# Kernel optimization log

Measured on AMD Instinct MI355X. Metric: run time of the kernel, lower is better.

The kernel has to match this reference:

```python
import jax, jax.numpy as jnp
import numpy as np

# config constants (match init_kwargs)
C = 1024
NH = 16
HS = C // NH
CHUNK = 64          # attn_chunk_size
TOPK = 32           # attn_topk
WINDOW = 4096       # kv_cache_window_size
MIN_KV = 16384      # min_kv_cache_size
MAX_KV = 32768      # max_kv_cache_size
SHORT = 4096        # short_sequence_criteria
CT = 65536          # incoming kv-cache length


def setup_inputs() -> dict:
    key = jax.random.key(0)
    ks = jax.random.split(key, 7)
    s = 1.0 / np.sqrt(C)
    return {
        "x": jax.random.normal(ks[0], (C,), jnp.float32),
        "k_cache": jax.random.normal(ks[1], (1, CT, C), jnp.float32),
        "v_cache": jax.random.normal(ks[2], (1, CT, C), jnp.float32),
        "Wr": jax.random.normal(ks[3], (C, C), jnp.float32) * s,
        "Wk": jax.random.normal(ks[4], (C, C), jnp.float32) * s,
        "Wv": jax.random.normal(ks[5], (C, C), jnp.float32) * s,
        "Wo": jax.random.normal(ks[6], (C, C), jnp.float32) * s,
    }


def _split_heads(t):  # (1, T, C) -> (1, NH, T, HS)
    return t.reshape(1, t.shape[1], NH, HS).transpose(0, 2, 1, 3)


def _update_kv_cache(q, k_cache, v_cache):
    # q: (1,1,C); caches: (1,CT,C). CT > MIN_KV so compression runs.
    past = CT - WINDOW
    kp = _split_heads(k_cache[:, :past])          # (1,NH,past,HS)
    vp = _split_heads(v_cache[:, :past])
    qh = _split_heads(q)                          # (1,NH,1,HS)
    scores = jnp.einsum("bhqd,bhkd->bhqk", qh, kp) / np.sqrt(HS)
    w = jax.nn.softmax(scores, axis=-1)           # (1,NH,1,past)
    vote = w.sum(axis=-2)                         # (1,NH,past)
    keep = MIN_KV - WINDOW                        # per-head tokens kept
    _, idx = jax.lax.top_k(vote, keep)            # (1,NH,keep), descending vote order
    kpc = jnp.take_along_axis(kp, idx[..., None], axis=2)  # (1,NH,keep,HS)
    vpc = jnp.take_along_axis(vp, idx[..., None], axis=2)
    kpc = kpc.transpose(0, 2, 1, 3).reshape(1, keep, C)
    vpc = vpc.transpose(0, 2, 1, 3).reshape(1, keep, C)
    k_new = jnp.concatenate([kpc, k_cache[:, past:]], axis=1)  # (1, MIN_KV, C)
    v_new = jnp.concatenate([vpc, v_cache[:, past:]], axis=1)
    return k_new, v_new


def reference(x, k_cache, v_cache, Wr, Wk, Wv, Wo):
    x2 = x[None, None, :]                         # (1,1,C)
    q = x2 @ Wr.T
    k = x2 @ Wk.T
    v = x2 @ Wv.T

    # CT > MAX_KV -> compress cache (eviction via attention vote per head)
    k_cache, v_cache = _update_kv_cache(q, k_cache, v_cache)
    CT2 = k_cache.shape[1]                        # MIN_KV = 16384 > SHORT -> sparse path

    num_chunks = CT2 // CHUNK
    kc = k_cache.reshape(1, num_chunks, CHUNK, C)
    vc = v_cache.reshape(1, num_chunks, CHUNK, C)
    chunk_key = kc.mean(axis=2)                   # (1,num_chunks,C)
    chunk_score = jnp.einsum("bqc,bkc->bqk", q, chunk_key)
    _, tidx = jax.lax.top_k(chunk_score[0, 0], TOPK)  # (TOPK,)
    topk_k = kc[:, tidx].reshape(1, TOPK * CHUNK, C)
    topk_v = vc[:, tidx].reshape(1, TOPK * CHUNK, C)

    k_comb = jnp.concatenate([topk_k, k], axis=1)  # (1, TOPK*CHUNK+1, C)
    v_comb = jnp.concatenate([topk_v, v], axis=1)

    qh = _split_heads(q)                          # (1,NH,1,HS)
    kh = _split_heads(k_comb)
    vh = _split_heads(v_comb)
    attn = jax.nn.softmax(
        jnp.einsum("bhqd,bhkd->bhqk", qh, kh) / np.sqrt(HS), axis=-1)
    y = jnp.einsum("bhqk,bhkd->bhqd", attn, vh)   # (1,NH,1,HS)
    y = y.transpose(0, 2, 1, 3).reshape(C)
    y = y @ Wo.T
    return y
```

## Files before the change

### kernel.cpp

```cpp
#include <hip/hip_runtime.h>
#include <stdint.h>

#define C      1024
#define NH     16
#define HS     64
#define CT     65536
#define PAST   61440
#define KEEP   12288
#define NCOMP  192
#define NSEL   32
#define NB     8192
#define NBLK   256
#define FLAGW  8

typedef unsigned long long ull;

#define LD_A(p)   __hip_atomic_load((p), __ATOMIC_RELAXED, __HIP_MEMORY_SCOPE_AGENT)
#define ST_A(p,v) __hip_atomic_store((p), (v), __ATOMIC_RELAXED, __HIP_MEMORY_SCOPE_AGENT)

__device__ __forceinline__ unsigned int desc_key(float f) {
    unsigned int b = __float_as_uint(f);
    return (b >> 31) ? b : (~b & 0x7FFFFFFFu);
}
__device__ __forceinline__ float u_to_f(unsigned int u) {
    unsigned int b = (u & 0x80000000u) ? u : (0x7FFFFFFFu - u);
    return __uint_as_float(b);
}
__device__ __forceinline__ int bin_of(float s, float hi, float scale) {
    int b = (int)((hi - s) * scale);
    return b < 0 ? 0 : (b > NB - 1 ? NB - 1 : b);
}
__device__ __forceinline__ void load_params(const unsigned* umin, const unsigned* umax,
                                            int h, float* hi, float* sc) {
    float h2 = u_to_f(umin[h]);
    float lo = u_to_f(umax[h]);
    float r = h2 - lo;
    *hi = h2;
    *sc = (r > 0.f) ? (float)(NB - 1) / r : 0.f;
}

__device__ __forceinline__ void arrive(unsigned* flag, unsigned ph) {
    __syncthreads();
    if (threadIdx.x == 0) {
        asm volatile("s_waitcnt vmcnt(0)" ::: "memory");
        ST_A(&flag[blockIdx.x * FLAGW], ph);
    }
}
__device__ __forceinline__ void wait_head(unsigned* flag, unsigned ph, int h) {
    if (threadIdx.x < 16)
        while (LD_A(&flag[(h * 16 + threadIdx.x) * FLAGW]) < ph)
            __builtin_amdgcn_s_sleep(2);
    __syncthreads();
}
__device__ __forceinline__ void wait_all(unsigned* flag, unsigned ph) {
    if (threadIdx.x < 256)
        while (LD_A(&flag[threadIdx.x * FLAGW]) < ph)
            __builtin_amdgcn_s_sleep(2);
    __syncthreads();
}

__global__ void k_proj(const float* __restrict__ x, const float* __restrict__ Wr,
                       const float* __restrict__ Wk, const float* __restrict__ Wv,
                       float* __restrict__ q, float* __restrict__ kn, float* __restrict__ vn,
                       unsigned* __restrict__ hc, unsigned* __restrict__ umin,
                       unsigned* __restrict__ umax, ull* __restrict__ cs_fix,
                       unsigned* __restrict__ flag) {
    int gid = blockIdx.x * 256 + threadIdx.x;
    for (int i = gid; i < 2 * NH * NB; i += 196608) hc[i] = 0;
    if (blockIdx.x >= 512 && blockIdx.x < 520)
        flag[(blockIdx.x - 512) * 256 + threadIdx.x] = 0u;
    if (blockIdx.x == 700) {
        if (threadIdx.x < 16) umin[threadIdx.x] = 0xFFFFFFFFu;
        else if (threadIdx.x < 32) umax[threadIdx.x - 16] = 0u;
    }
    if (blockIdx.x == 701 && threadIdx.x < 256) cs_fix[threadIdx.x] = 0ull;

    int w = blockIdx.x * (blockDim.x >> 6) + (threadIdx.x >> 6);
    int lane = threadIdx.x & 63;
    int mat = w >> 10, row = w & 1023;
    const float* W = (mat == 0) ? Wr : (mat == 1) ? Wk : Wv;
    const float4* Wrow = (const float4*)(W + (size_t)row * C);
    const float4* x4 = (const float4*)x;
    float acc = 0.f;
#pragma unroll
    for (int i = 0; i < 4; ++i) {
        float4 a = Wrow[i * 64 + lane];
        float4 b = x4[i * 64 + lane];
        acc += a.x * b.x + a.y * b.y + a.z * b.z + a.w * b.w;
    }
#pragma unroll
    for (int off = 32; off; off >>= 1) acc += __shfl_xor(acc, off);
    if (lane == 0) { (mat == 0 ? q : (mat == 1 ? kn : vn))[row] = acc; }
}

__global__ void k_scores(const float* __restrict__ kc, const float* __restrict__ q,
                         float* __restrict__ s, unsigned* __restrict__ umin,
                         unsigned* __restrict__ umax, ull* __restrict__ cs_fix) {
    __shared__ float sc_l[4][16][17];
    __shared__ float smn[4][16], smx[4][16];
    __shared__ long long wred[4];
    int wave = threadIdx.x >> 6, lane = threadIdx.x & 63;
    int wid = blockIdx.x * 4 + wave;
    int t0 = wid * 16;
    const float4* q4 = (const float4*)q;
    float4 qv[4];
#pragma unroll
    for (int i = 0; i < 4; ++i) qv[i] = q4[i * 64 + lane];
    float mnv[4] = {3.4e38f, 3.4e38f, 3.4e38f, 3.4e38f};
    float mxv[4] = {-3.4e38f, -3.4e38f, -3.4e38f, -3.4e38f};
    for (int tt = 0; tt < 16; ++tt) {
        const float4* row = (const float4*)(kc + (size_t)(t0 + tt) * C);
        float acc[4];
#pragma unroll
        for (int i = 0; i < 4; ++i) {
            float4 a = row[i * 64 + lane];
            acc[i] = a.x * qv[i].x + a.y * qv[i].y + a.z * qv[i].z + a.w * qv[i].w;
        }
#pragma unroll
        for (int off = 8; off; off >>= 1) {
#pragma unroll
            for (int i = 0; i < 4; ++i) acc[i] += __shfl_xor(acc[i], off);
        }
        if ((lane & 15) == 0) {
            int g = lane >> 4;
#pragma unroll
            for (int i = 0; i < 4; ++i) {
                sc_l[wave][4 * i + g][tt] = acc[i];
                mnv[i] = fminf(mnv[i], acc[i]);
                mxv[i] = fmaxf(mxv[i], acc[i]);
            }
        }
    }
    __syncthreads();
    int tt2 = lane & 15;
#pragma unroll
    for (int r = 0; r < 4; ++r) {
        int h = r * 4 + (lane >> 4);
        s[(size_t)h * CT + t0 + tt2] = sc_l[wave][h][tt2];
    }
    if (blockIdx.x < 960) {
        if ((lane & 15) == 0) {
            int g = lane >> 4;
#pragma unroll
            for (int i = 0; i < 4; ++i) { smn[wave][4 * i + g] = mnv[i]; smx[wave][4 * i + g] = mxv[i]; }
        }
        __syncthreads();
        if (threadIdx.x < 16) {
            int h = threadIdx.x;
            float mn = smn[0][h], mx = smx[0][h];
            for (int w2 = 1; w2 < 4; ++w2) {
                mn = fminf(mn, smn[w2][h]);
                mx = fmaxf(mx, smx[w2][h]);
            }
            atomicMin(&umin[h], desc_key(mx));
            atomicMax(&umax[h], desc_key(mn));
        }
    } else {
        int hh = threadIdx.x >> 4, tt = threadIdx.x & 15;
        long long f = 0;
#pragma unroll
        for (int w2 = 0; w2 < 4; ++w2) f += llrintf(sc_l[w2][hh][tt] * 16777216.f);
#pragma unroll
        for (int off = 32; off; off >>= 1) f += __shfl_xor(f, off);
        if (lane == 0) wred[wave] = f;
        __syncthreads();
        if (threadIdx.x == 0)
            cs_fix[NCOMP + (blockIdx.x - 960)] =
                (ull)(wred[0] + wred[1] + wred[2] + wred[3]);
    }
}

__global__ __launch_bounds__(1024, 2) void k_mega(
        const float* __restrict__ s, const float* __restrict__ vc,
        const unsigned* __restrict__ umin, const unsigned* __restrict__ umax,
        unsigned* __restrict__ hist, unsigned* __restrict__ cnt,
        ull* __restrict__ G, unsigned* __restrict__ stok,
        ull* __restrict__ cs_fix, float* __restrict__ part,
        const float* __restrict__ q, const float* __restrict__ kn,
        const float* __restrict__ vn, const float* __restrict__ Wo,
        float* __restrict__ yg, float* __restrict__ out,
        unsigned* __restrict__ flag) {
    const int bid = blockIdx.x, tid = threadIdx.x;
    const int lane = tid & 63, wave = tid >> 6;
    const int h = bid >> 4, seg = bid & 15;
    __shared__ __align__(16) char smem[40960];
    __shared__ unsigned shT, shN;
    __shared__ unsigned wsum[16];

    float hi, sc; load_params(umin, umax, h, &hi, &sc);
    unsigned* lh = (unsigned*)smem;

    {
        for (int i = tid; i < NB; i += 1024) lh[i] = 0;
        __syncthreads();
        const float* sh = s + (size_t)h * CT + seg * 3840;
        for (int i = tid; i < 3840; i += 1024)
            atomicAdd(&lh[bin_of(sh[i], hi, sc)], 1u);
        __syncthreads();
        unsigned* gh = hist + h * NB;
        for (int i = tid; i < NB; i += 1024) {
            unsigned c = lh[i];
            if (c) atomicAdd(&gh[i], c);
        }
    }
    arrive(flag, 1); wait_head(flag, 1, h);

    {
        const unsigned* gh = hist + h * NB;
        unsigned c8[8]; unsigned loc = 0; int b0 = tid * 8;
#pragma unroll
        for (int k = 0; k < 8; ++k) { c8[k] = gh[b0 + k]; loc += c8[k]; }
        unsigned run = loc;
#pragma unroll
        for (int off = 1; off < 64; off <<= 1) {
            unsigned n = __shfl_up(run, off);
            if (lane >= off) run += n;
        }
        if (lane == 63) wsum[wave] = run;
        __syncthreads();
        if (wave == 0 && lane < 16) {
            unsigned v = wsum[lane];
#pragma unroll
            for (int off = 1; off < 16; off <<= 1) {
                unsigned n = __shfl_up(v, off);
                if (lane >= off) v += n;
            }
            wsum[lane] = v;
        }
        __syncthreads();
        unsigned r = run - loc + (wave ? wsum[wave - 1] : 0u);
#pragma unroll
        for (int k = 0; k < 8; ++k) {
            unsigned c = c8[k];
            lh[b0 + k] = r;
            unsigned inc = r + c;
            if (r < KEEP && inc >= KEEP) { shT = (unsigned)(b0 + k); shN = inc; }
            r = inc;
        }
    }
    __syncthreads();
    const unsigned T = shT, ncand = shN;

    {
        const float* sh = s + (size_t)h * CT + seg * 3840;
        unsigned* ch = cnt + h * NB;
        ull* Gh = G + (size_t)h * 65536;
        for (int i = tid; i < 3840; i += 1024) {
            float v = sh[i];
            int b = bin_of(v, hi, sc);
            if ((unsigned)b <= T) {
                unsigned pos = lh[b] + atomicAdd(&ch[b], 1u);
                ST_A(&Gh[pos], ((ull)desc_key(v) << 16) | (unsigned)(seg * 3840 + i));
            }
        }
    }
    arrive(flag, 2); wait_head(flag, 2, h);

    {
        ull* csl = (ull*)(smem + 32768);
        if (tid < NCOMP) csl[tid] = 0ull;
        __syncthreads();
        const ull* Gh = G + (size_t)h * 65536;
        for (unsigned p = seg * 1024 + tid; p < ncand; p += 16384) {
            ull pk = Gh[p];
            unsigned u = (unsigned)(pk >> 16);
            float v = u_to_f(u);
            int b = bin_of(v, hi, sc);
            unsigned start = lh[b];
            unsigned end = (b == NB - 1) ? ncand : lh[b + 1];
            unsigned rank = start;
            for (unsigned j = start; j < end; ++j) rank += (Gh[j] < pk) ? 1u : 0u;
            if (rank < KEEP) {
                ST_A(&stok[h * KEEP + rank], (unsigned)(pk & 0xFFFFull));
                long long f = llrintf(v * 16777216.f);
                atomicAdd(&csl[rank >> 6], (ull)f);
            }
        }
        __syncthreads();
        if (tid < NCOMP) {
            ull c = csl[tid];
            if (c) atomicAdd(&cs_fix[tid], c);
        }
    }
    arrive(flag, 3); wait_all(flag, 3);

    {
        ull* key = (ull*)smem;
        unsigned* sel_l = (unsigned*)(smem + 2048);
        float* scm = (float*)(smem + 2176);
        float* exb = (float*)(smem + 2688);
        float* vbuf = (float*)(smem + 3200);
        if (tid < 256) {
            long long v = (long long)cs_fix[tid];
            ull bb = (ull)(v + (1ll << 45));
            key[tid] = (((1ull << 46) - bb) << 8) | (unsigned)tid;
        }
        __syncthreads();
        for (unsigned k = 2; k <= 256; k <<= 1) {
            for (unsigned j = k >> 1; j > 0; j >>= 1) {
                if (tid < 256) {
                    unsigned ixj = tid ^ j;
                    if (ixj > (unsigned)tid) {
                        ull a = key[tid], b = key[ixj];
                        bool up = ((tid & k) == 0);
                        if (up ? (a > b) : (a < b)) { key[tid] = b; key[ixj] = a; }
                    }
                }
                __syncthreads();
            }
        }
        if (tid < NSEL) sel_l[tid] = (unsigned)(key[tid] & 0xFFull);
        __syncthreads();

        int su = tid >> 9, sid = tid & 511;
        int p = bid * 2 + su;
        int hh = p >> 5, ci = p & 31;
        int c = (int)sel_l[ci];
        int g = sid >> 3, q8 = sid & 7;
        int t = (c < NCOMP) ? (int)stok[hh * KEEP + c * 64 + g]
                            : (PAST + (c - NCOMP) * 64 + g);
        if (q8 == 0) scm[su * 64 + g] = s[(size_t)hh * CT + t] * 0.125f;
        __syncthreads();
        float m = -1e30f;
        for (int j = 0; j < 64; ++j) m = fmaxf(m, scm[su * 64 + j]);
        float e = expf(scm[su * 64 + g] - m);
        if (q8 == 0) exb[su * 64 + g] = e;
        const float4* vrow = (const float4*)(vc + (size_t)t * C + hh * HS);
        float4 v0 = vrow[q8 * 2], v1 = vrow[q8 * 2 + 1];
        float* vb = vbuf + su * 4352 + g * 68 + q8 * 8;
        vb[0] = e * v0.x; vb[1] = e * v0.y; vb[2] = e * v0.z; vb[3] = e * v0.w;
        vb[4] = e * v1.x; vb[5] = e * v1.y; vb[6] = e * v1.z; vb[7] = e * v1.w;
        __syncthreads();
        if (sid < 64) {
            float acc = 0.f;
            for (int g2 = 0; g2 < 64; ++g2) acc += vbuf[su * 4352 + g2 * 68 + sid];
            float* P = part + (size_t)(hh * 32 + ci) * 68;
            ST_A(&P[2 + sid], acc);
            if (sid == 0) {
                float es = 0.f;
                for (int g2 = 0; g2 < 64; ++g2) es += exb[su * 64 + g2];
                ST_A(&P[0], m);
                ST_A(&P[1], es);
            }
        }
    }
    arrive(flag, 4); wait_head(flag, 4, h);

    if (seg == 0 && tid < 64) {
        float p = q[h * 64 + tid] * kn[h * 64 + tid];
#pragma unroll
        for (int off = 32; off; off >>= 1) p += __shfl_xor(p, off);
        float a_new = p * 0.125f;
        const float* P0 = part + (size_t)h * 32 * 68;
        float m = a_new;
        for (int ci = 0; ci < 32; ++ci) m = fmaxf(m, P0[ci * 68]);
        float den = expf(a_new - m);
        float acc = den * vn[h * HS + tid];
        for (int ci = 0; ci < 32; ++ci) {
            float w = expf(P0[ci * 68] - m);
            den += w * P0[ci * 68 + 1];
            acc += w * P0[ci * 68 + 2 + tid];
        }
        ST_A(&yg[h * HS + tid], acc / den);
    }
    arrive(flag, 5); wait_all(flag, 5);

    {
        float* yl = (float*)smem;
        float* ps = (float*)(smem + 4096);
        yl[tid] = yg[tid];
        __syncthreads();
        int row = bid * 4 + (wave >> 2), qtr = wave & 3;
        const float4* Wrow = (const float4*)(Wo + (size_t)row * C) + qtr * 64;
        const float4* y4 = (const float4*)yl + qtr * 64;
        float4 a = Wrow[lane], b = y4[lane];
        float acc = a.x * b.x + a.y * b.y + a.z * b.z + a.w * b.w;
#pragma unroll
        for (int off = 32; off; off >>= 1) acc += __shfl_xor(acc, off);
        if (lane == 0) ps[wave] = acc;
        __syncthreads();
        if (tid < 4)
            out[bid * 4 + tid] = ps[tid * 4] + ps[tid * 4 + 1] + ps[tid * 4 + 2] + ps[tid * 4 + 3];
    }
}

extern "C" void kernel_launch(void* const* d_in, const int* in_sizes, int n_in,
                              void* d_out, int out_size, void* d_ws, size_t ws_size,
                              hipStream_t stream) {
    const float* x  = (const float*)d_in[0];
    const float* kc = (const float*)d_in[1];
    const float* vc = (const float*)d_in[2];
    const float* Wr = (const float*)d_in[3];
    const float* Wk = (const float*)d_in[4];
    const float* Wv = (const float*)d_in[5];
    const float* Wo = (const float*)d_in[6];
    float* out = (float*)d_out;
    char* ws = (char*)d_ws;

    float* q    = (float*)(ws + 0);
    float* kn   = (float*)(ws + 8192);
    float* vn   = (float*)(ws + 16384);
    ull* cs_fix = (ull*)(ws + 32768);
    float* yg   = (float*)(ws + 40960);
    float* part = (float*)(ws + 49152);
    unsigned* stok = (unsigned*)(ws + 196608);
    unsigned* umin = (unsigned*)(ws + 1048576);
    unsigned* umax = (unsigned*)(ws + 1048640);
    unsigned* flag = (unsigned*)(ws + 1048832);
    unsigned* hist = (unsigned*)(ws + 1114112);
    unsigned* cnt  = (unsigned*)(ws + 1638400);
    float* s = (float*)(ws + 2621440);
    ull* G = (ull*)(ws + 7340032);

    k_proj<<<768, 256, 0, stream>>>(x, Wr, Wk, Wv, q, kn, vn, hist, umin, umax, cs_fix, flag);
    k_scores<<<1024, 256, 0, stream>>>(kc, q, s, umin, umax, cs_fix);
    k_mega<<<NBLK, 1024, 0, stream>>>(s, vc, umin, umax, hist, cnt, G, stok, cs_fix,
                                      part, q, kn, vn, Wo, yg, out, flag);
}
```

Measured before the change: 124.0 us.

## Fuse score computation into persistent mega kernel and cache scores in LDS

The separate k_scores launch is folded into the persistent k_mega kernel. Each of the 256 blocks (1024 threads) now computes 256 token scores, publishes min/max and the chunk sums, and then hits a new grid-wide barrier before histogramming. Each block also keeps its 3840-score segment in shared memory, so the candidate-scatter pass reads LDS instead of re-reading global memory. This removes one kernel launch and a global re-read, at the cost of an extra grid-wide sync and more LDS per block, which may lower occupancy.

Result: faster. 119.2 us (-3.9%).

```diff
diff --git a/kernel.cpp b/kernel.cpp
--- a/kernel.cpp
+++ b/kernel.cpp
@@ -93,109 +93,115 @@
     if (lane == 0) { (mat == 0 ? q : (mat == 1 ? kn : vn))[row] = acc; }
 }
 
-__global__ void k_scores(const float* __restrict__ kc, const float* __restrict__ q,
-                         float* __restrict__ s, unsigned* __restrict__ umin,
-                         unsigned* __restrict__ umax, ull* __restrict__ cs_fix) {
-    __shared__ float sc_l[4][16][17];
-    __shared__ float smn[4][16], smx[4][16];
-    __shared__ long long wred[4];
-    int wave = threadIdx.x >> 6, lane = threadIdx.x & 63;
-    int wid = blockIdx.x * 4 + wave;
-    int t0 = wid * 16;
-    const float4* q4 = (const float4*)q;
-    float4 qv[4];
-#pragma unroll
-    for (int i = 0; i < 4; ++i) qv[i] = q4[i * 64 + lane];
-    float mnv[4] = {3.4e38f, 3.4e38f, 3.4e38f, 3.4e38f};
-    float mxv[4] = {-3.4e38f, -3.4e38f, -3.4e38f, -3.4e38f};
-    for (int tt = 0; tt < 16; ++tt) {
-        const float4* row = (const float4*)(kc + (size_t)(t0 + tt) * C);
-        float acc[4];
-#pragma unroll
-        for (int i = 0; i < 4; ++i) {
-            float4 a = row[i * 64 + lane];
-            acc[i] = a.x * qv[i].x + a.y * qv[i].y + a.z * qv[i].z + a.w * qv[i].w;
-        }
-#pragma unroll
-        for (int off = 8; off; off >>= 1) {
-#pragma unroll
-            for (int i = 0; i < 4; ++i) acc[i] += __shfl_xor(acc[i], off);
-        }
-        if ((lane & 15) == 0) {
-            int g = lane >> 4;
-#pragma unroll
-            for (int i = 0; i < 4; ++i) {
-                sc_l[wave][4 * i + g][tt] = acc[i];
-                mnv[i] = fminf(mnv[i], acc[i]);
-                mxv[i] = fmaxf(mxv[i], acc[i]);
-            }
-        }
-    }
-    __syncthreads();
-    int tt2 = lane & 15;
-#pragma unroll
-    for (int r = 0; r < 4; ++r) {
-        int h = r * 4 + (lane >> 4);
-        s[(size_t)h * CT + t0 + tt2] = sc_l[wave][h][tt2];
-    }
-    if (blockIdx.x < 960) {
-        if ((lane & 15) == 0) {
-            int g = lane >> 4;
-#pragma unroll
-            for (int i = 0; i < 4; ++i) { smn[wave][4 * i + g] = mnv[i]; smx[wave][4 * i + g] = mxv[i]; }
-        }
-        __syncthreads();
-        if (threadIdx.x < 16) {
-            int h = threadIdx.x;
-            float mn = smn[0][h], mx = smx[0][h];
-            for (int w2 = 1; w2 < 4; ++w2) {
-                mn = fminf(mn, smn[w2][h]);
-                mx = fmaxf(mx, smx[w2][h]);
-            }
-            atomicMin(&umin[h], desc_key(mx));
-            atomicMax(&umax[h], desc_key(mn));
-        }
-    } else {
-        int hh = threadIdx.x >> 4, tt = threadIdx.x & 15;
-        long long f = 0;
-#pragma unroll
-        for (int w2 = 0; w2 < 4; ++w2) f += llrintf(sc_l[w2][hh][tt] * 16777216.f);
-#pragma unroll
-        for (int off = 32; off; off >>= 1) f += __shfl_xor(f, off);
-        if (lane == 0) wred[wave] = f;
-        __syncthreads();
-        if (threadIdx.x == 0)
-            cs_fix[NCOMP + (blockIdx.x - 960)] =
-                (ull)(wred[0] + wred[1] + wred[2] + wred[3]);
-    }
-}
-
 __global__ __launch_bounds__(1024, 2) void k_mega(
-        const float* __restrict__ s, const float* __restrict__ vc,
-        const unsigned* __restrict__ umin, const unsigned* __restrict__ umax,
+        const float* __restrict__ kc, const float* __restrict__ s_dummy,
+        const float* __restrict__ vc,
+        unsigned* __restrict__ umin, unsigned* __restrict__ umax,
         unsigned* __restrict__ hist, unsigned* __restrict__ cnt,
         ull* __restrict__ G, unsigned* __restrict__ stok,
         ull* __restrict__ cs_fix, float* __restrict__ part,
         const float* __restrict__ q, const float* __restrict__ kn,
         const float* __restrict__ vn, const float* __restrict__ Wo,
         float* __restrict__ yg, float* __restrict__ out,
-        unsigned* __restrict__ flag) {
+        float* __restrict__ s, unsigned* __restrict__ flag) {
     const int bid = blockIdx.x, tid = threadIdx.x;
     const int lane = tid & 63, wave = tid >> 6;
     const int h = bid >> 4, seg = bid & 15;
-    __shared__ __align__(16) char smem[40960];
+    __shared__ __align__(16) char smem[49664];
     __shared__ unsigned shT, shN;
     __shared__ unsigned wsum[16];
+    __shared__ long long wredl[16];
+
+    {
+        float (*scl)[16][17] = (float(*)[16][17])smem;
+        float* smn = (float*)(smem + 18496);
+        float* smx = (float*)(smem + 19520);
+        const int t0 = bid * 256 + wave * 16;
+        const float4* q4 = (const float4*)q;
+        float4 qv[4];
+#pragma unroll
+        for (int i = 0; i < 4; ++i) qv[i] = q4[i * 64 + lane];
+        float mnv[4] = {3.4e38f, 3.4e38f, 3.4e38f, 3.4e38f};
+        float mxv[4] = {-3.4e38f, -3.4e38f, -3.4e38f, -3.4e38f};
+        for (int tt = 0; tt < 16; ++tt) {
+            const float4* row = (const float4*)(kc + (size_t)(t0 + tt) * C);
+            float acc[4];
+#pragma unroll
+            for (int i = 0; i < 4; ++i) {
+                float4 a = row[i * 64 + lane];
+                acc[i] = a.x * qv[i].x + a.y * qv[i].y + a.z * qv[i].z + a.w * qv[i].w;
+            }
+#pragma unroll
+            for (int off = 8; off; off >>= 1) {
+#pragma unroll
+                for (int i = 0; i < 4; ++i) acc[i] += __shfl_xor(acc[i], off);
+            }
+            if ((lane & 15) == 0) {
+                int g = lane >> 4;
+#pragma unroll
+                for (int i = 0; i < 4; ++i) {
+                    scl[wave][4 * i + g][tt] = acc[i];
+                    mnv[i] = fminf(mnv[i], acc[i]);
+                    mxv[i] = fmaxf(mxv[i], acc[i]);
+                }
+            }
+        }
+        __syncthreads();
+        int tt2 = lane & 15;
+#pragma unroll
+        for (int r = 0; r < 4; ++r) {
+            int h2 = r * 4 + (lane >> 4);
+            ST_A(&s[(size_t)h2 * CT + t0 + tt2], scl[wave][h2][tt2]);
+        }
+        if (bid < 240) {
+            if ((lane & 15) == 0) {
+                int g = lane >> 4;
+#pragma unroll
+                for (int i = 0; i < 4; ++i) {
+                    smn[wave * 16 + 4 * i + g] = mnv[i];
+                    smx[wave * 16 + 4 * i + g] = mxv[i];
+                }
+            }
+            __syncthreads();
+            if (tid < 16) {
+                float mn = smn[tid], mx = smx[tid];
+                for (int w2 = 1; w2 < 16; ++w2) {
+                    mn = fminf(mn, smn[w2 * 16 + tid]);
+                    mx = fmaxf(mx, smx[w2 * 16 + tid]);
+                }
+                atomicMin(&umin[tid], desc_key(mx));
+                atomicMax(&umax[tid], desc_key(mn));
+            }
+        } else {
+            int k = tid >> 8, sub = tid & 255, hh = sub >> 4, tt = sub & 15;
+            long long f = 0;
+#pragma unroll
+            for (int w2 = 0; w2 < 4; ++w2)
+                f += llrintf(scl[4 * k + w2][hh][tt] * 16777216.f);
+#pragma unroll
+            for (int off = 32; off; off >>= 1) f += __shfl_xor(f, off);
+            if ((tid & 63) == 0) wredl[wave] = f;
+            __syncthreads();
+            if ((tid & 255) == 0)
+                ST_A(&cs_fix[NCOMP + (bid - 240) * 4 + k],
+                     (ull)(wredl[4 * k] + wredl[4 * k + 1] + wredl[4 * k + 2] + wredl[4 * k + 3]));
+        }
+    }
+    arrive(flag, 1); wait_all(flag, 1);
 
     float hi, sc; load_params(umin, umax, h, &hi, &sc);
     unsigned* lh = (unsigned*)smem;
+    float* s_local = (float*)(smem + 32768);
 
     {
         for (int i = tid; i < NB; i += 1024) lh[i] = 0;
         __syncthreads();
         const float* sh = s + (size_t)h * CT + seg * 3840;
-        for (int i = tid; i < 3840; i += 1024)
-            atomicAdd(&lh[bin_of(sh[i], hi, sc)], 1u);
+        for (int i = tid; i < 3840; i += 1024) {
+            float v = sh[i];
+            s_local[i] = v;
+            atomicAdd(&lh[bin_of(v, hi, sc)], 1u);
+        }
         __syncthreads();
         unsigned* gh = hist + h * NB;
         for (int i = tid; i < NB; i += 1024) {
@@ -203,7 +209,7 @@
             if (c) atomicAdd(&gh[i], c);
         }
     }
-    arrive(flag, 1); wait_head(flag, 1, h);
+    arrive(flag, 2); wait_head(flag, 2, h);
 
     {
         const unsigned* gh = hist + h * NB;
@@ -242,11 +248,10 @@
     const unsigned T = shT, ncand = shN;
 
     {
-        const float* sh = s + (size_t)h * CT + seg * 3840;
         unsigned* ch = cnt + h * NB;
         ull* Gh = G + (size_t)h * 65536;
         for (int i = tid; i < 3840; i += 1024) {
-            float v = sh[i];
+            float v = s_local[i];
             int b = bin_of(v, hi, sc);
             if ((unsigned)b <= T) {
                 unsigned pos = lh[b] + atomicAdd(&ch[b], 1u);
@@ -254,10 +259,10 @@
             }
         }
     }
-    arrive(flag, 2); wait_head(flag, 2, h);
-
-    {
-        ull* csl = (ull*)(smem + 32768);
+    arrive(flag, 3); wait_head(flag, 3, h);
+
+    {
+        ull* csl = (ull*)(smem + 48128);
         if (tid < NCOMP) csl[tid] = 0ull;
         __syncthreads();
         const ull* Gh = G + (size_t)h * 65536;
@@ -282,7 +287,7 @@
             if (c) atomicAdd(&cs_fix[tid], c);
         }
     }
-    arrive(flag, 3); wait_all(flag, 3);
+    arrive(flag, 4); wait_all(flag, 4);
 
     {
         ull* key = (ull*)smem;
@@ -344,7 +349,7 @@
             }
         }
     }
-    arrive(flag, 4); wait_head(flag, 4, h);
+    arrive(flag, 5); wait_head(flag, 5, h);
 
     if (seg == 0 && tid < 64) {
         float p = q[h * 64 + tid] * kn[h * 64 + tid];
@@ -363,7 +368,7 @@
         }
         ST_A(&yg[h * HS + tid], acc / den);
     }
-    arrive(flag, 5); wait_all(flag, 5);
+    arrive(flag, 6); wait_all(flag, 6);
 
     {
         float* yl = (float*)smem;
@@ -413,7 +418,6 @@
     ull* G = (ull*)(ws + 7340032);
 
     k_proj<<<768, 256, 0, stream>>>(x, Wr, Wk, Wv, q, kn, vn, hist, umin, umax, cs_fix, flag);
-    k_scores<<<1024, 256, 0, stream>>>(kc, q, s, umin, umax, cs_fix);
-    k_mega<<<NBLK, 1024, 0, stream>>>(s, vc, umin, umax, hist, cnt, G, stok, cs_fix,
-                                      part, q, kn, vn, Wo, yg, out, flag);
-}
+    k_mega<<<NBLK, 1024, 0, stream>>>(kc, s, vc, umin, umax, hist, cnt, G, stok, cs_fix,
+                                      part, q, kn, vn, Wo, yg, out, s, flag);
+}
```
